# Kernel optimization log

Hardware: AMD Instinct MI355X
Metric: run time of the kernel (lower is better)

## Reference

```python
import jax, jax.numpy as jnp
import numpy as np

NUM_USER = 100000
NUM_ITEM = 50000
N = NUM_USER + NUM_ITEM
E = 1200000
D = 64          # emb_size
F_ITEM = 384    # raw item multimodal feature dim
K = 3           # number of global embedding rows (summed over dim 0)
N_LAYERS = 4
EPS = 1e-8      # F.cosine_similarity default eps


def setup_inputs() -> dict:
    key = jax.random.key(0)
    ks = jax.random.split(key, 9)
    return {
        "adj_row": jax.random.randint(ks[0], (E,), 0, N),
        "adj_col": jax.random.randint(ks[1], (E,), 0, N),
        # scaled like a degree-normalized adjacency (avg degree ~8)
        "adj_val": jax.random.uniform(ks[2], (E,), jnp.float32) / 8.0,
        "user_fea": jax.random.normal(ks[3], (NUM_USER, D), jnp.float32) * 0.1,
        "item_fea": jax.random.normal(ks[4], (NUM_ITEM, F_ITEM), jnp.float32) * 0.1,
        "g_emb_u": jax.random.normal(ks[5], (K, D), jnp.float32) * 0.1,
        "g_emb_i": jax.random.normal(ks[6], (K, D), jnp.float32) * 0.1,
        "mlp_w": jax.random.normal(ks[7], (D, F_ITEM), jnp.float32) * (1.0 / np.sqrt(F_ITEM)),
        "mlp_b": jnp.zeros((D,), jnp.float32),
    }


def _cosine_sim(a, b):
    # matches F.cosine_similarity(a, b, dim=-1) with eps clamp on norms
    na = jnp.maximum(jnp.linalg.norm(a, axis=-1), EPS)
    nb = jnp.maximum(jnp.linalg.norm(b, axis=-1), EPS)
    return jnp.sum(a * b, axis=-1) / (na * nb)


def reference(adj_row, adj_col, adj_val, user_fea, item_fea, g_emb_u, g_emb_i, mlp_w, mlp_b):
    # global embeddings summed over modality dim
    user_emb = user_fea + jnp.sum(g_emb_u, axis=0)                       # [U, D]
    item_emb = jnp.tanh(item_fea @ mlp_w.T + mlp_b) + jnp.sum(g_emb_i, axis=0)  # [I, D]
    ego = jnp.concatenate([user_emb, item_emb], axis=0)                  # [N, D]

    x = ego
    acc = ego  # sum over layers, includes layer-0 (ego) term
    for _ in range(N_LAYERS):
        # sparse adj @ x as gather -> scale -> segment-sum scatter
        x = jax.ops.segment_sum(adj_val[:, None] * x[adj_col], adj_row, num_segments=N)
        w = _cosine_sim(x, ego)     # [N]
        x = w[:, None] * x          # einsum('a,ab->ab')
        acc = acc + x

    return acc[:NUM_USER], acc[NUM_USER:]
```

## Files before the change

kernel.cpp:

```cpp
#include <hip/hip_runtime.h>
#include <hip/hip_bf16.h>

#define U_NUM 100000
#define I_NUM 50000
#define N_NUM 150000
#define E_NUM 1200000
#define D 64
#define F_IT 384
#define CAP 32
#define EPSV 1e-8f
#define FXS 524288.0f
#define FXI (1.0f / 524288.0f)

#define NBIN 586
#define RPB 256
#define FBLK 586
#define CELL_CAP 8
#define OV_CAP 256

typedef unsigned short ushort_t;
typedef unsigned int uint_t;
typedef short bf16x8 __attribute__((ext_vector_type(8)));
typedef float f32x4 __attribute__((ext_vector_type(4)));

__device__ __forceinline__ ushort_t f2bf(float f) {
    uint_t x = __float_as_uint(f);
    uint_t r = x + 0x7fffu + ((x >> 16) & 1u);
    return (ushort_t)(r >> 16);
}
__device__ __forceinline__ float bfu2f(uint_t u_lo16) {
    return __uint_as_float(u_lo16 << 16);
}
__device__ __forceinline__ void dec8(uint4 u, float* f) {
    f[0] = bfu2f(u.x & 0xffffu); f[1] = bfu2f(u.x >> 16);
    f[2] = bfu2f(u.y & 0xffffu); f[3] = bfu2f(u.y >> 16);
    f[4] = bfu2f(u.z & 0xffffu); f[5] = bfu2f(u.z >> 16);
    f[6] = bfu2f(u.w & 0xffffu); f[7] = bfu2f(u.w >> 16);
}

__global__ void k_prep(const float* __restrict__ w, const float* __restrict__ gu,
                       const float* __restrict__ gi,
                       short* __restrict__ wbf, float* __restrict__ gsu,
                       float* __restrict__ gsi, int* __restrict__ ovcnt) {
    int b = blockIdx.x, t = threadIdx.x;
    if (b < 96) {
        int i = b * 256 + t;
        wbf[i] = (short)f2bf(w[i]);
    } else {
        if (t < 64) gsu[t] = gu[t] + gu[64 + t] + gu[128 + t];
        else if (t < 128) { int d = t - 64; gsi[d] = gi[d] + gi[64 + d] + gi[128 + d]; }
        for (int i = t; i < NBIN; i += 256) ovcnt[i] = 0;
    }
}

__global__ __launch_bounds__(256) void k_fill(
        const int* __restrict__ row, const int* __restrict__ col,
        const float* __restrict__ val,
        int2* __restrict__ cellbuf, int* __restrict__ cellcnt,
        int* __restrict__ ovcnt, int2* __restrict__ ovbuf) {
    __shared__ int bincnt[NBIN];
    int fid = blockIdx.x, tid = threadIdx.x;
    for (int i = tid; i < NBIN; i += 256) bincnt[i] = 0;
    __syncthreads();
    int t = fid * 256 + tid;
    if (t < E_NUM / 8) {
        int r[8], c[8];
        float v[8];
#pragma unroll
        for (int k = 0; k < 8; k++) {
            int e = k * (E_NUM / 8) + t;
            r[k] = row[e]; c[k] = col[e]; v[k] = val[e];
        }
#pragma unroll
        for (int k = 0; k < 8; k++) {
            int bn = r[k] >> 8;
            int key = c[k] | ((r[k] & 255) << 18);
            int ls = atomicAdd(&bincnt[bn], 1);
            if (ls < CELL_CAP) {
                cellbuf[((size_t)fid * NBIN + bn) * CELL_CAP + ls] =
                    make_int2(key, __float_as_int(v[k]));
            } else {
                int o = atomicAdd(&ovcnt[bn], 1);
                if (o < OV_CAP) ovbuf[bn * OV_CAP + o] = make_int2(key, __float_as_int(v[k]));
            }
        }
    }
    __syncthreads();
    for (int i = tid; i < NBIN; i += 256)
        cellcnt[(size_t)fid * NBIN + i] = min(bincnt[i], CELL_CAP);
}

#define ITEM_B 782
__global__ __launch_bounds__(256, 3) void k_item(
        const float* __restrict__ ifea, const float* __restrict__ bvec,
        const short* __restrict__ wbf, const float* __restrict__ gsi,
        float* __restrict__ ego, ushort_t* __restrict__ egob) {
    int iid = blockIdx.x;
    int tid = threadIdx.x;
    int wave = tid >> 6, lane = tid & 63;
    int q = lane >> 4, m = lane & 15;
    int ibase = iid * 64 + wave * 16;
    int irow = min(ibase + m, I_NUM - 1);
    const float* arow = ifea + (size_t)irow * F_IT + q * 8;

    float4 fa[12][2];
#pragma unroll
    for (int c = 0; c < 12; c++) {
        fa[c][0] = ((const float4*)(arow + c * 32))[0];
        fa[c][1] = ((const float4*)(arow + c * 32))[1];
    }
    __builtin_amdgcn_sched_barrier(0);

    f32x4 av[4];
#pragma unroll
    for (int n = 0; n < 4; n++) av[n] = (f32x4){0.f, 0.f, 0.f, 0.f};
#pragma unroll
    for (int c = 0; c < 12; c++) {
        bf16x8 af;
        af[0] = (short)f2bf(fa[c][0].x); af[1] = (short)f2bf(fa[c][0].y);
        af[2] = (short)f2bf(fa[c][0].z); af[3] = (short)f2bf(fa[c][0].w);
        af[4] = (short)f2bf(fa[c][1].x); af[5] = (short)f2bf(fa[c][1].y);
        af[6] = (short)f2bf(fa[c][1].z); af[7] = (short)f2bf(fa[c][1].w);
#pragma unroll
        for (int n = 0; n < 4; n++) {
            bf16x8 bf = *(const bf16x8*)(wbf + (size_t)(n * 16 + m) * F_IT + c * 32 + q * 8);
            av[n] = __builtin_amdgcn_mfma_f32_16x16x32_bf16(af, bf, av[n], 0, 0, 0);
        }
    }
#pragma unroll
    for (int n = 0; n < 4; n++) {
        int dim = n * 16 + m;
        float bb = bvec[dim];
        float gg = gsi[dim];
#pragma unroll
        for (int rr = 0; rr < 4; rr++) {
            int item = ibase + q * 4 + rr;
            if (item < I_NUM) {
                float v = tanhf(av[n][rr] + bb) + gg;
                size_t o = (size_t)(U_NUM + item) * D + dim;
                ego[o] = v;
                egob[o] = f2bf(v);
            }
        }
    }
}

#define USER_B 1563
__global__ __launch_bounds__(256) void k_user(
        const float* __restrict__ ufea, const float* __restrict__ gsu,
        float* __restrict__ ego, ushort_t* __restrict__ egob) {
    int t = blockIdx.x * 256 + threadIdx.x;
    size_t base = (size_t)t * 16;
    if (base >= (size_t)U_NUM * D) return;
    int d0 = (int)(base & 63);
    float f[16];
#pragma unroll
    for (int k = 0; k < 4; k++) {
        float4 v = ((const float4*)(ufea + base))[k];
        f[4 * k] = v.x; f[4 * k + 1] = v.y; f[4 * k + 2] = v.z; f[4 * k + 3] = v.w;
    }
#pragma unroll
    for (int j = 0; j < 16; j++) f[j] += gsu[d0 + j];
#pragma unroll
    for (int k = 0; k < 4; k++) {
        ((float4*)(ego + base))[k] = make_float4(f[4 * k], f[4 * k + 1], f[4 * k + 2], f[4 * k + 3]);
    }
    uint4 u0, u1;
    u0.x = (uint_t)f2bf(f[0]) | ((uint_t)f2bf(f[1]) << 16);
    u0.y = (uint_t)f2bf(f[2]) | ((uint_t)f2bf(f[3]) << 16);
    u0.z = (uint_t)f2bf(f[4]) | ((uint_t)f2bf(f[5]) << 16);
    u0.w = (uint_t)f2bf(f[6]) | ((uint_t)f2bf(f[7]) << 16);
    u1.x = (uint_t)f2bf(f[8]) | ((uint_t)f2bf(f[9]) << 16);
    u1.y = (uint_t)f2bf(f[10]) | ((uint_t)f2bf(f[11]) << 16);
    u1.z = (uint_t)f2bf(f[12]) | ((uint_t)f2bf(f[13]) << 16);
    u1.w = (uint_t)f2bf(f[14]) | ((uint_t)f2bf(f[15]) << 16);
    ((uint4*)(egob + base))[0] = u0;
    ((uint4*)(egob + base))[1] = u1;
}

__global__ __launch_bounds__(256) void k_bucket(const int2* __restrict__ cellbuf,
                                                const int* __restrict__ cellcnt,
                                                const int* __restrict__ ovcnt,
                                                const int2* __restrict__ ovbuf,
                                                int* __restrict__ cnt,
                                                int2* __restrict__ bkt) {
    __shared__ int lc[RPB];
    int bn = blockIdx.x, tid = threadIdx.x;
    lc[tid] = 0;
    __syncthreads();
    int rbase = bn << 8;
#pragma unroll
    for (int h = 0; h < 3; h++) {
        int f = h * 256 + tid;
        if (f < FBLK) {
            int c = cellcnt[(size_t)f * NBIN + bn];
            const int2* cp = cellbuf + ((size_t)f * NBIN + bn) * CELL_CAP;
            for (int i = 0; i < c; i++) {
                int2 e = cp[i];
                int rl = e.x >> 18;
                int s = atomicAdd(&lc[rl], 1);
                if (s < CAP) bkt[(size_t)(rbase + rl) * CAP + s] = make_int2(e.x & 0x3ffff, e.y);
            }
        }
    }
    int oc = min(ovcnt[bn], OV_CAP);
    for (int i = tid; i < oc; i += 256) {
        int2 e = ovbuf[bn * OV_CAP + i];
        int rl = e.x >> 18;
        int s = atomicAdd(&lc[rl], 1);
        if (s < CAP) bkt[(size_t)(rbase + rl) * CAP + s] = make_int2(e.x & 0x3ffff, e.y);
    }
    __syncthreads();
    int r = rbase + tid;
    if (r < N_NUM) {
        int d = min(lc[tid], CAP);
        int dp = (d <= 16) ? 16 : 32;
        for (int s = d; s < dp; s++)
            bkt[(size_t)r * CAP + s] = make_int2(0, 0);
        cnt[r] = dp;
    }
}

#define ACC8(A, VS, X) \
    A[0] += __float2int_rn(VS * bfu2f(X.x & 0xffffu)); A[1] += __float2int_rn(VS * bfu2f(X.x >> 16)); \
    A[2] += __float2int_rn(VS * bfu2f(X.y & 0xffffu)); A[3] += __float2int_rn(VS * bfu2f(X.y >> 16)); \
    A[4] += __float2int_rn(VS * bfu2f(X.z & 0xffffu)); A[5] += __float2int_rn(VS * bfu2f(X.z >> 16)); \
    A[6] += __float2int_rn(VS * bfu2f(X.w & 0xffffu)); A[7] += __float2int_rn(VS * bfu2f(X.w >> 16));

__device__ __forceinline__ float row_weight(const float* a, const float* e) {
    float dot = 0.f, nx = 0.f, ne = 0.f;
#pragma unroll
    for (int j = 0; j < 8; j++) {
        dot += a[j] * e[j]; nx += a[j] * a[j]; ne += e[j] * e[j];
    }
#pragma unroll
    for (int m = 1; m < 8; m <<= 1) {
        dot += __shfl_xor(dot, m);
        nx  += __shfl_xor(nx, m);
        ne  += __shfl_xor(ne, m);
    }
    return dot / (fmaxf(sqrtf(nx), EPSV) * fmaxf(sqrtf(ne), EPSV));
}

__device__ __forceinline__ void gather_row(const ushort_t* __restrict__ xb,
                                           const int2* __restrict__ bp,
                                           int dp, int l, int* __restrict__ a) {
#pragma unroll
    for (int j = 0; j < 8; j++) a[j] = 0;
    const int4* cp = (const int4*)bp;
    int4 p[8];
#pragma unroll
    for (int j = 0; j < 8; j++) p[j] = cp[j];
    uint4 xu[16];
#pragma unroll
    for (int j = 0; j < 8; j++) {
        xu[2 * j]     = ((const uint4*)xb)[(size_t)p[j].x * 8 + l];
        xu[2 * j + 1] = ((const uint4*)xb)[(size_t)p[j].z * 8 + l];
    }
    __builtin_amdgcn_sched_barrier(0);
#pragma unroll
    for (int j = 0; j < 8; j++) {
        float va = __int_as_float(p[j].y) * FXS;
        float vb = __int_as_float(p[j].w) * FXS;
        ACC8(a, va, xu[2 * j]);
        ACC8(a, vb, xu[2 * j + 1]);
    }
    if (dp > 16) {
#pragma unroll
        for (int k = 2; k < 4; k++) {
            int4 q01 = cp[4 * k + 0], q23 = cp[4 * k + 1];
            int4 q45 = cp[4 * k + 2], q67 = cp[4 * k + 3];
            uint4 yu[8];
            yu[0] = ((const uint4*)xb)[(size_t)q01.x * 8 + l];
            yu[1] = ((const uint4*)xb)[(size_t)q01.z * 8 + l];
            yu[2] = ((const uint4*)xb)[(size_t)q23.x * 8 + l];
            yu[3] = ((const uint4*)xb)[(size_t)q23.z * 8 + l];
            yu[4] = ((const uint4*)xb)[(size_t)q45.x * 8 + l];
            yu[5] = ((const uint4*)xb)[(size_t)q45.z * 8 + l];
            yu[6] = ((const uint4*)xb)[(size_t)q67.x * 8 + l];
            yu[7] = ((const uint4*)xb)[(size_t)q67.z * 8 + l];
            float w0 = __int_as_float(q01.y) * FXS, w1 = __int_as_float(q01.w) * FXS;
            float w2 = __int_as_float(q23.y) * FXS, w3 = __int_as_float(q23.w) * FXS;
            float w4 = __int_as_float(q45.y) * FXS, w5 = __int_as_float(q45.w) * FXS;
            float w6 = __int_as_float(q67.y) * FXS, w7 = __int_as_float(q67.w) * FXS;
            ACC8(a, w0, yu[0]); ACC8(a, w1, yu[1]);
            ACC8(a, w2, yu[2]); ACC8(a, w3, yu[3]);
            ACC8(a, w4, yu[4]); ACC8(a, w5, yu[5]);
            ACC8(a, w6, yu[6]); ACC8(a, w7, yu[7]);
        }
    }
}

__device__ __forceinline__ void spmm_body(const ushort_t* __restrict__ xb,
                                          const ushort_t* __restrict__ egob,
                                          const int* __restrict__ cnt,
                                          const int2* __restrict__ bkt,
                                          ushort_t* __restrict__ xob) {
    int t = blockIdx.x * 256 + threadIdx.x;
    int l = t & 7, r = t >> 3;
    if (r >= N_NUM) return;
    int dp = cnt[r];
    int a[8];
    gather_row(xb, bkt + (size_t)r * CAP, dp, l, a);
    float af[8];
#pragma unroll
    for (int j = 0; j < 8; j++) af[j] = (float)a[j] * FXI;
    float e[8]; dec8(((const uint4*)egob)[(size_t)r * 8 + l], e);
    float wgt = row_weight(af, e);
    uint4 ov;
    ov.x = (uint_t)f2bf(wgt * af[0]) | ((uint_t)f2bf(wgt * af[1]) << 16);
    ov.y = (uint_t)f2bf(wgt * af[2]) | ((uint_t)f2bf(wgt * af[3]) << 16);
    ov.z = (uint_t)f2bf(wgt * af[4]) | ((uint_t)f2bf(wgt * af[5]) << 16);
    ov.w = (uint_t)f2bf(wgt * af[6]) | ((uint_t)f2bf(wgt * af[7]) << 16);
    ((uint4*)xob)[(size_t)r * 8 + l] = ov;
}

__global__ __launch_bounds__(256, 4) void k_spmmA(const ushort_t* __restrict__ xb,
        const ushort_t* __restrict__ egob, const int* __restrict__ cnt,
        const int2* __restrict__ bkt, ushort_t* __restrict__ xob)
{ spmm_body(xb, egob, cnt, bkt, xob); }

__global__ __launch_bounds__(256, 4) void k_spmmB(const ushort_t* __restrict__ xb,
        const ushort_t* __restrict__ egob, const int* __restrict__ cnt,
        const int2* __restrict__ bkt, ushort_t* __restrict__ xob)
{ spmm_body(xb, egob, cnt, bkt, xob); }

__global__ __launch_bounds__(256, 4) void k_spmmC(const ushort_t* __restrict__ xb,
        const ushort_t* __restrict__ egob, const int* __restrict__ cnt,
        const int2* __restrict__ bkt, ushort_t* __restrict__ xob)
{ spmm_body(xb, egob, cnt, bkt, xob); }

__global__ __launch_bounds__(256, 4) void k_spmm4(const ushort_t* __restrict__ x3,
                                                  const ushort_t* __restrict__ x1,
                                                  const ushort_t* __restrict__ x2,
                                                  const float* __restrict__ ego,
                                                  const int* __restrict__ cnt,
                                                  const int2* __restrict__ bkt,
                                                  float* __restrict__ out) {
    int t = blockIdx.x * 256 + threadIdx.x;
    int l = t & 7, r = t >> 3;
    if (r >= N_NUM) return;
    int dp = cnt[r];
    int a[8];
    gather_row(x3, bkt + (size_t)r * CAP, dp, l, a);
    float af[8];
#pragma unroll
    for (int j = 0; j < 8; j++) af[j] = (float)a[j] * FXI;
    size_t rb = (size_t)r * D + l * 8;
    float e[8];
    float4 e0 = ((const float4*)(ego + rb))[0];
    float4 e1 = ((const float4*)(ego + rb))[1];
    e[0] = e0.x; e[1] = e0.y; e[2] = e0.z; e[3] = e0.w;
    e[4] = e1.x; e[5] = e1.y; e[6] = e1.z; e[7] = e1.w;
    float wgt = row_weight(af, e);
    float x1d[8], x2d[8], x3d[8];
    dec8(((const uint4*)x1)[(size_t)r * 8 + l], x1d);
    dec8(((const uint4*)x2)[(size_t)r * 8 + l], x2d);
    dec8(((const uint4*)x3)[(size_t)r * 8 + l], x3d);
    float s[8];
#pragma unroll
    for (int j = 0; j < 8; j++) s[j] = e[j] + x1d[j] + x2d[j] + x3d[j] + wgt * af[j];
    ((float4*)(out + rb))[0] = make_float4(s[0], s[1], s[2], s[3]);
    ((float4*)(out + rb))[1] = make_float4(s[4], s[5], s[6], s[7]);
}

extern "C" void kernel_launch(void* const* d_in, const int* in_sizes, int n_in,
                              void* d_out, int out_size, void* d_ws, size_t ws_size,
                              hipStream_t stream) {
    const int*   adj_row  = (const int*)d_in[0];
    const int*   adj_col  = (const int*)d_in[1];
    const float* adj_val  = (const float*)d_in[2];
    const float* user_fea = (const float*)d_in[3];
    const float* item_fea = (const float*)d_in[4];
    const float* gu       = (const float*)d_in[5];
    const float* gi       = (const float*)d_in[6];
    const float* mlp_w    = (const float*)d_in[7];
    const float* mlp_b    = (const float*)d_in[8];

    float* out = (float*)d_out;

    char* ws = (char*)d_ws;
    size_t off = 0;
    float*    ego  = (float*)(ws + off);    off += (size_t)N_NUM * D * 4;
    ushort_t* egob = (ushort_t*)(ws + off); off += (size_t)N_NUM * D * 2;
    size_t x1off = off;
    ushort_t* x1   = (ushort_t*)(ws + off); off += (size_t)N_NUM * D * 2;
    ushort_t* x2   = (ushort_t*)(ws + off); off += (size_t)N_NUM * D * 2;
    ushort_t* x3   = (ushort_t*)(ws + off); off += (size_t)N_NUM * D * 2;
    int*      cnt  = (int*)(ws + off);      off += (size_t)N_NUM * 4;
    short*    wbf  = (short*)(ws + off);    off += (size_t)D * F_IT * 2;
    float*    gsu  = (float*)(ws + off);    off += 64 * 4;
    float*    gsi  = (float*)(ws + off);    off += 64 * 4;
    off = (off + 255) & ~(size_t)255;
    int2*     bkt  = (int2*)(ws + off);     off += (size_t)N_NUM * CAP * 8;
    int*      cellcnt = (int*)(ws + off);   off += (size_t)FBLK * NBIN * 4;
    int*      ovcnt   = (int*)(ws + off);   off += (size_t)NBIN * 4;
    int2*     ovbuf   = (int2*)(ws + off);  off += (size_t)NBIN * OV_CAP * 8;
    int2*     cellbuf = (int2*)(ws + x1off);

    k_prep<<<97, 256, 0, stream>>>(mlp_w, gu, gi, wbf, gsu, gsi, ovcnt);
    k_fill<<<FBLK, 256, 0, stream>>>(adj_row, adj_col, adj_val,
                                     cellbuf, cellcnt, ovcnt, ovbuf);
    k_item<<<ITEM_B, 256, 0, stream>>>(item_fea, mlp_b, wbf, gsi, ego, egob);
    k_user<<<USER_B, 256, 0, stream>>>(user_fea, gsu, ego, egob);
    k_bucket<<<NBIN, 256, 0, stream>>>(cellbuf, cellcnt, ovcnt, ovbuf, cnt, bkt);
    int g = ((size_t)N_NUM * 8 + 255) / 256;
    k_spmmA<<<g, 256, 0, stream>>>(egob, egob, cnt, bkt, x1);
    k_spmmB<<<g, 256, 0, stream>>>(x1,   egob, cnt, bkt, x2);
    k_spmmC<<<g, 256, 0, stream>>>(x2,   egob, cnt, bkt, x3);
    k_spmm4<<<g, 256, 0, stream>>>(x3, x1, x2, ego, cnt, bkt, out);
}
```

Baseline: 389.9 us.

## Split item MLP K-dimension across wave pairs with LDS reduction

The item projection kernel now gives each 16-row tile to two waves, each covering half of the 384-wide reduction, and the partial accumulators are combined through shared memory. Each wave then writes two of the four output column groups. The full register preload of the input row is replaced by a one-step software prefetch, and the occupancy hint of 3 is dropped. This doubles the block count and cuts per-wave register pressure and serial MFMA chain length, at the cost of an LDS exchange and a block barrier.

```diff
diff --git a/kernel.cpp b/kernel.cpp
--- a/kernel.cpp
+++ b/kernel.cpp
@@ -90,45 +90,53 @@
         cellcnt[(size_t)fid * NBIN + i] = min(bincnt[i], CELL_CAP);
 }
 
-#define ITEM_B 782
-__global__ __launch_bounds__(256, 3) void k_item(
+#define ITEM_B 1563
+__global__ __launch_bounds__(256) void k_item(
         const float* __restrict__ ifea, const float* __restrict__ bvec,
         const short* __restrict__ wbf, const float* __restrict__ gsi,
         float* __restrict__ ego, ushort_t* __restrict__ egob) {
-    int iid = blockIdx.x;
-    int tid = threadIdx.x;
+    __shared__ f32x4 xch[2][2][64][2];
+    int iid = blockIdx.x, tid = threadIdx.x;
     int wave = tid >> 6, lane = tid & 63;
+    int tile = wave >> 1, half = wave & 1;
     int q = lane >> 4, m = lane & 15;
-    int ibase = iid * 64 + wave * 16;
+    int ibase = iid * 32 + tile * 16;
     int irow = min(ibase + m, I_NUM - 1);
     const float* arow = ifea + (size_t)irow * F_IT + q * 8;
 
-    float4 fa[12][2];
-#pragma unroll
-    for (int c = 0; c < 12; c++) {
-        fa[c][0] = ((const float4*)(arow + c * 32))[0];
-        fa[c][1] = ((const float4*)(arow + c * 32))[1];
-    }
-    __builtin_amdgcn_sched_barrier(0);
-
     f32x4 av[4];
 #pragma unroll
     for (int n = 0; n < 4; n++) av[n] = (f32x4){0.f, 0.f, 0.f, 0.f};
-#pragma unroll
-    for (int c = 0; c < 12; c++) {
+    int c0 = half * 6;
+    float4 nfa0 = ((const float4*)(arow + c0 * 32))[0];
+    float4 nfa1 = ((const float4*)(arow + c0 * 32))[1];
+#pragma unroll
+    for (int cc = 0; cc < 6; cc++) {
+        int c = c0 + cc;
+        float4 fa0 = nfa0, fa1 = nfa1;
+        if (cc < 5) {
+            nfa0 = ((const float4*)(arow + (c + 1) * 32))[0];
+            nfa1 = ((const float4*)(arow + (c + 1) * 32))[1];
+        }
         bf16x8 af;
-        af[0] = (short)f2bf(fa[c][0].x); af[1] = (short)f2bf(fa[c][0].y);
-        af[2] = (short)f2bf(fa[c][0].z); af[3] = (short)f2bf(fa[c][0].w);
-        af[4] = (short)f2bf(fa[c][1].x); af[5] = (short)f2bf(fa[c][1].y);
-        af[6] = (short)f2bf(fa[c][1].z); af[7] = (short)f2bf(fa[c][1].w);
+        af[0] = (short)f2bf(fa0.x); af[1] = (short)f2bf(fa0.y);
+        af[2] = (short)f2bf(fa0.z); af[3] = (short)f2bf(fa0.w);
+        af[4] = (short)f2bf(fa1.x); af[5] = (short)f2bf(fa1.y);
+        af[6] = (short)f2bf(fa1.z); af[7] = (short)f2bf(fa1.w);
 #pragma unroll
         for (int n = 0; n < 4; n++) {
             bf16x8 bf = *(const bf16x8*)(wbf + (size_t)(n * 16 + m) * F_IT + c * 32 + q * 8);
             av[n] = __builtin_amdgcn_mfma_f32_16x16x32_bf16(af, bf, av[n], 0, 0, 0);
         }
     }
-#pragma unroll
-    for (int n = 0; n < 4; n++) {
+    int oth = 2 * (1 - half);
+    xch[tile][half][lane][0] = av[oth];
+    xch[tile][half][lane][1] = av[oth + 1];
+    __syncthreads();
+#pragma unroll
+    for (int k = 0; k < 2; k++) {
+        int n = 2 * half + k;
+        f32x4 s = av[n] + xch[tile][1 - half][lane][k];
         int dim = n * 16 + m;
         float bb = bvec[dim];
         float gg = gsi[dim];
@@ -136,7 +144,7 @@
         for (int rr = 0; rr < 4; rr++) {
             int item = ibase + q * 4 + rr;
             if (item < I_NUM) {
-                float v = tanhf(av[n][rr] + bb) + gg;
+                float v = tanhf(s[rr] + bb) + gg;
                 size_t o = (size_t)(U_NUM + item) * D + dim;
                 ego[o] = v;
                 egob[o] = f2bf(v);
```

Result: no change. 385.3 us (-1.2%).

## Double-buffer item feature tiles into LDS via direct global-to-LDS loads

Applied to the files above, without the earlier changes.

The item MLP kernel used to load its whole 384-float feature row slice into registers up front. It now stages one 32-column chunk at a time into a double-buffered LDS array using global_load_lds, so the load of the next chunk overlaps the MFMA work on the current one. This cuts register pressure, which is why the occupancy hint in the launch bounds is dropped. The cost is a __syncthreads per chunk and extra LDS traffic. The staging and read index mapping has to match the MFMA operand layout exactly.

```diff
diff --git a/kernel.cpp b/kernel.cpp
--- a/kernel.cpp
+++ b/kernel.cpp
@@ -91,42 +91,58 @@
 }
 
 #define ITEM_B 782
-__global__ __launch_bounds__(256, 3) void k_item(
+__global__ __launch_bounds__(256) void k_item(
         const float* __restrict__ ifea, const float* __restrict__ bvec,
         const short* __restrict__ wbf, const float* __restrict__ gsi,
         float* __restrict__ ego, ushort_t* __restrict__ egob) {
-    int iid = blockIdx.x;
-    int tid = threadIdx.x;
+    __shared__ float ab[2][2048];
+    int iid = blockIdx.x, tid = threadIdx.x;
     int wave = tid >> 6, lane = tid & 63;
     int q = lane >> 4, m = lane & 15;
     int ibase = iid * 64 + wave * 16;
-    int irow = min(ibase + m, I_NUM - 1);
-    const float* arow = ifea + (size_t)irow * F_IT + q * 8;
-
-    float4 fa[12][2];
+
+    int sq0 = tid >> 7;
+    int sr  = (tid >> 1) & 63;
+    int sf  = (tid & 1) * 4;
+    int sirow = min(iid * 64 + sr, I_NUM - 1);
+    const float* g0 = ifea + (size_t)sirow * F_IT + (sq0 * 2 + 0) * 0;
+
+#define STAGE(cc, buf) do {                                                        \
+        _Pragma("unroll")                                                          \
+        for (int p = 0; p < 2; p++) {                                              \
+            int qq = p * 2 + sq0;                                                  \
+            const float* gsrc = ifea + (size_t)sirow * F_IT + (cc) * 32 + qq * 8 + sf; \
+            float* ldst = &ab[buf][0] + p * 1024 + tid * 4;                        \
+            __builtin_amdgcn_global_load_lds(                                      \
+                (const __attribute__((address_space(1))) void*)gsrc,               \
+                (__attribute__((address_space(3))) void*)ldst, 16, 0, 0);          \
+        }                                                                          \
+    } while (0)
+
+    f32x4 av[4];
+#pragma unroll
+    for (int n = 0; n < 4; n++) av[n] = (f32x4){0.f, 0.f, 0.f, 0.f};
+
+    STAGE(0, 0);
 #pragma unroll
     for (int c = 0; c < 12; c++) {
-        fa[c][0] = ((const float4*)(arow + c * 32))[0];
-        fa[c][1] = ((const float4*)(arow + c * 32))[1];
-    }
-    __builtin_amdgcn_sched_barrier(0);
-
-    f32x4 av[4];
-#pragma unroll
-    for (int n = 0; n < 4; n++) av[n] = (f32x4){0.f, 0.f, 0.f, 0.f};
-#pragma unroll
-    for (int c = 0; c < 12; c++) {
+        __syncthreads();
+        if (c < 11) STAGE(c + 1, (c + 1) & 1);
+        const float* src = &ab[c & 1][0] + q * 512 + (wave * 16 + m) * 8;
+        float4 fa0 = ((const float4*)src)[0];
+        float4 fa1 = ((const float4*)src)[1];
         bf16x8 af;
-        af[0] = (short)f2bf(fa[c][0].x); af[1] = (short)f2bf(fa[c][0].y);
-        af[2] = (short)f2bf(fa[c][0].z); af[3] = (short)f2bf(fa[c][0].w);
-        af[4] = (short)f2bf(fa[c][1].x); af[5] = (short)f2bf(fa[c][1].y);
-        af[6] = (short)f2bf(fa[c][1].z); af[7] = (short)f2bf(fa[c][1].w);
+        af[0] = (short)f2bf(fa0.x); af[1] = (short)f2bf(fa0.y);
+        af[2] = (short)f2bf(fa0.z); af[3] = (short)f2bf(fa0.w);
+        af[4] = (short)f2bf(fa1.x); af[5] = (short)f2bf(fa1.y);
+        af[6] = (short)f2bf(fa1.z); af[7] = (short)f2bf(fa1.w);
 #pragma unroll
         for (int n = 0; n < 4; n++) {
             bf16x8 bf = *(const bf16x8*)(wbf + (size_t)(n * 16 + m) * F_IT + c * 32 + q * 8);
             av[n] = __builtin_amdgcn_mfma_f32_16x16x32_bf16(af, bf, av[n], 0, 0, 0);
         }
     }
+#undef STAGE
 #pragma unroll
     for (int n = 0; n < 4; n++) {
         int dim = n * 16 + m;
@@ -143,6 +159,7 @@
             }
         }
     }
+    (void)g0;
 }
 
 #define USER_B 1563
```

New measurement: 386.2 us. Within noise of the previous version (-1.0%).
